# Performance work log

Hardware: AMD Instinct MI355X
Metric: run time of the kernel (lower is better)

## Reference

```python
import jax, jax.numpy as jnp
import numpy as np

K, N = 8192, 8192
GROUP_SIZE = 128
N_GROUPS = N // GROUP_SIZE  # 64
NBITS = 4
B, T = 8, 32


def setup_inputs() -> dict:
    key = jax.random.key(0)
    k_x, k_q, k_s, k_z, k_m1, k_m2, k_b = jax.random.split(key, 7)
    x = jax.random.normal(k_x, (B, T, N), dtype=jnp.float32)
    # int8 quantized weight codes in [0, 2**nbits - 1]
    W_q = jax.random.randint(k_q, (K, N), 0, 2 ** NBITS, dtype=jnp.int32)
    # group-wise scales/zeros, shaped for broadcast against [K, n_groups, group_size]
    scales = jax.random.uniform(k_s, (K, N_GROUPS, 1), dtype=jnp.float32, minval=0.01, maxval=0.1)
    zeros = jax.random.uniform(k_z, (K, N_GROUPS, 1), dtype=jnp.float32, minval=0.0, maxval=2.0 ** NBITS - 1.0)
    # Sinkhorn row/col scaling factors (positive, near 1)
    mu1 = jnp.exp(0.1 * jax.random.normal(k_m1, (N,), dtype=jnp.float32))
    mu2 = jnp.exp(0.1 * jax.random.normal(k_m2, (K,), dtype=jnp.float32))
    bias = jax.random.normal(k_b, (K,), dtype=jnp.float32)
    return {"x": x, "W_q": W_q, "scales": scales, "zeros": zeros,
            "mu1": mu1, "mu2": mu2, "bias": bias}


def reference(x, W_q, scales, zeros, mu1, mu2, bias):
    k, n = W_q.shape
    n_groups = scales.shape[1]
    group_size = n // n_groups
    # group-wise dequant: (Q - zero) * scale, then Sinkhorn row/col rescale
    Q_g = W_q.astype(jnp.float32).reshape(k, n_groups, group_size)
    W_deq = ((Q_g - zeros) * scales).reshape(k, n)
    W_deq = W_deq * mu2[:, None] * mu1[None, :]
    W_deq = W_deq.astype(x.dtype)
    # nn.functional.linear: x @ W^T + b ; x: [B, T, N] -> [B, T, K]
    out = jnp.einsum('btn,kn->btk', x, W_deq) + bias
    return out
```

## Files before the change

kernel.cpp:

```cpp
#include <hip/hip_runtime.h>
#include <hip/hip_bf16.h>

#define M_DIM 256
#define K_DIM 8192
#define N_DIM 8192
#define NGRP  64

#define BN 128
#define BK 32
#define THREADS 512
#define SPLITN 8
#define CHUNK  (N_DIM / SPLITN)
#define NSTEPS (CHUNK / BK)
#define NG     (CHUNK >> 7)

#define ASIZE 16384
#define BSIZE 8192
#define B_OFF  (3 * ASIZE)
#define SL_OFF (B_OFF + 2 * BSIZE)
#define LDS_TOTAL (SL_OFF + NG * 128 * 8)

typedef __bf16 bf16x8 __attribute__((ext_vector_type(8)));
typedef __bf16 bf16x4 __attribute__((ext_vector_type(4)));
typedef float  f32x4  __attribute__((ext_vector_type(4)));

#define SW(a) ((a) ^ ((((a) >> 7) & 7) << 4))

#define GLOAD_LDS16(g, l) __builtin_amdgcn_global_load_lds( \
    (const __attribute__((address_space(1))) void*)(g),     \
    (__attribute__((address_space(3))) void*)(l), 16, 0, 0)

__global__ __launch_bounds__(256) void prep_xs(const float* __restrict__ x,
                                               const float* __restrict__ mu1,
                                               __bf16* __restrict__ xs) {
    int t  = blockIdx.x * 256 + threadIdx.x;
    int n4 = t & 2047;
    int m  = t >> 11;
    int n  = n4 << 2;
    float4 xv = *(const float4*)(x + (size_t)m * N_DIM + n);
    float4 mv = *(const float4*)(mu1 + n);
    bf16x4 o;
    o[0] = (__bf16)(xv.x * mv.x);
    o[1] = (__bf16)(xv.y * mv.y);
    o[2] = (__bf16)(xv.z * mv.z);
    o[3] = (__bf16)(xv.w * mv.w);
    *(bf16x4*)(xs + (size_t)m * N_DIM + n) = o;
}

__global__ __launch_bounds__(THREADS, 4)
void gemm_q(const __bf16* __restrict__ xs, const int* __restrict__ Wq,
            const float* __restrict__ scales, const float* __restrict__ zeros,
            __bf16* __restrict__ partial) {
    extern __shared__ __align__(1024) char lds[];

    const int b     = blockIdx.x;
    const int split = b & 7;
    const int kidx  = b >> 3;
    const int k0    = kidx * BN;
    const int nbase = split * CHUNK;
    const int gbase = split * NG;

    const int tid  = threadIdx.x;
    const int lane = tid & 63;
    const int w    = tid >> 6;
    const int wmq  = w >> 1;
    const int wnh  = w & 1;
    const int start = kidx & (NSTEPS - 1);

    float* SL = (float*)(lds + SL_OFF);

    {
        int r = tid >> 2, gq = tid & 3;
#pragma unroll
        for (int gg = 0; gg < (NG >> 2); ++gg) {
            int g = (gg << 2) | gq;
            size_t si = (size_t)(k0 + r) * NGRP + gbase + g;
            float s = scales[si];
            float z = zeros[si];
            float2 v; v.x = s; v.y = -z * s;
            *(float2*)&SL[(size_t)((g << 7) + r) * 2] = v;
        }
    }
    asm volatile("s_waitcnt vmcnt(0) lgkmcnt(0)" ::: "memory");
    __builtin_amdgcn_s_barrier();

    const char* asrc[2];
    int aoff[2];
#pragma unroll
    for (int cc = 0; cc < 2; ++cc) {
        int c   = w * 2 + cc;
        int off = c * 1024 + lane * 16;
        int L   = SW(off);
        aoff[cc] = off;
        asrc[cc] = (const char*)xs + ((size_t)(L >> 6) * N_DIM) * 2 + (L & 63);
    }

    const int brow = w * 16 + (lane >> 2);
    const int bq   = lane & 3;
    const int* bptr0 = Wq + (size_t)(k0 + brow) * N_DIM + bq * 8;
    char* bdst0 = lds + B_OFF + SW(brow * 64 + bq * 16);

    int rb[4], ra[4];
#pragma unroll
    for (int i = 0; i < 4; ++i) {
        rb[i] = SW((wnh * 64 + i * 16 + (lane & 15)) * 64 + (lane >> 4) * 16);
        ra[i] = SW((wmq * 64 + i * 16 + (lane & 15)) * 64 + (lane >> 4) * 16);
    }

    char* pA0 = lds;
    char* pA1 = lds + ASIZE;
    char* pA2 = lds + 2 * ASIZE;

#define ISSUE_A(t, pbuf)                                                  \
    {                                                                     \
        int s_ = ((t) + start) & (NSTEPS - 1);                            \
        size_t so_ = (size_t)(nbase + s_ * BK) * 2;                       \
        GLOAD_LDS16(asrc[0] + so_, (pbuf) + aoff[0]);                     \
        GLOAD_LDS16(asrc[1] + so_, (pbuf) + aoff[1]);                     \
    }
#define LOAD_B(t, q0, q1)                                                 \
    {                                                                     \
        int s_ = ((t) + start) & (NSTEPS - 1);                            \
        const int* p_ = bptr0 + (nbase + s_ * BK);                        \
        q0 = *(const int4*)p_;                                            \
        q1 = *(const int4*)(p_ + 4);                                      \
    }

    f32x4 acc[4][4];
#pragma unroll
    for (int i = 0; i < 4; ++i)
#pragma unroll
        for (int j = 0; j < 4; ++j)
            acc[i][j] = (f32x4){0.f, 0.f, 0.f, 0.f};

    int4 qa0, qa1, qb0, qb1;

    LOAD_B(0, qa0, qa1);
    asm volatile("" ::: "memory");
    ISSUE_A(0, pA0);
    asm volatile("" ::: "memory");
    LOAD_B(1, qb0, qb1);
    asm volatile("" ::: "memory");
    ISSUE_A(1, pA1);

#define STEP(it, q0c, q1c, W1N, DO_ISS)                                   \
    {                                                                     \
        asm volatile("s_waitcnt vmcnt(" #W1N ")" ::: "memory");           \
        int scur_ = ((it) + start) & (NSTEPS - 1);                        \
        float2 sz_ = *(float2*)&SL[(size_t)(((scur_ >> 2) << 7) + brow) * 2]; \
        bf16x8 wv_;                                                       \
        wv_[0] = (__bf16)((float)q0c.x * sz_.x + sz_.y);                  \
        wv_[1] = (__bf16)((float)q0c.y * sz_.x + sz_.y);                  \
        wv_[2] = (__bf16)((float)q0c.z * sz_.x + sz_.y);                  \
        wv_[3] = (__bf16)((float)q0c.w * sz_.x + sz_.y);                  \
        wv_[4] = (__bf16)((float)q1c.x * sz_.x + sz_.y);                  \
        wv_[5] = (__bf16)((float)q1c.y * sz_.x + sz_.y);                  \
        wv_[6] = (__bf16)((float)q1c.z * sz_.x + sz_.y);                  \
        wv_[7] = (__bf16)((float)q1c.w * sz_.x + sz_.y);                  \
        *(bf16x8*)(bdst0 + ((it) & 1) * BSIZE) = wv_;                     \
        if (DO_ISS) { LOAD_B((it) + 2, q0c, q1c); }                       \
        asm volatile("s_waitcnt lgkmcnt(0)" ::: "memory");                \
        __builtin_amdgcn_s_barrier();                                     \
        const char* bufB_ = lds + B_OFF + ((it) & 1) * BSIZE;             \
        bf16x8 bv0_ = *(const bf16x8*)(bufB_ + rb[0]);                    \
        bf16x8 bv1_ = *(const bf16x8*)(bufB_ + rb[1]);                    \
        bf16x8 bv2_ = *(const bf16x8*)(bufB_ + rb[2]);                    \
        bf16x8 bv3_ = *(const bf16x8*)(bufB_ + rb[3]);                    \
        if (DO_ISS) { ISSUE_A((it) + 2, pA2); }                           \
        __builtin_amdgcn_s_setprio(1);                                    \
        _Pragma("unroll")                                                 \
        for (int mi = 0; mi < 4; ++mi) {                                  \
            bf16x8 av_ = *(const bf16x8*)(pA0 + ra[mi]);                  \
            acc[mi][0] = __builtin_amdgcn_mfma_f32_16x16x32_bf16(av_, bv0_, acc[mi][0], 0, 0, 0); \
            acc[mi][1] = __builtin_amdgcn_mfma_f32_16x16x32_bf16(av_, bv1_, acc[mi][1], 0, 0, 0); \
            acc[mi][2] = __builtin_amdgcn_mfma_f32_16x16x32_bf16(av_, bv2_, acc[mi][2], 0, 0, 0); \
            acc[mi][3] = __builtin_amdgcn_mfma_f32_16x16x32_bf16(av_, bv3_, acc[mi][3], 0, 0, 0); \
        }                                                                 \
        __builtin_amdgcn_s_setprio(0);                                    \
        { char* t_ = pA0; pA0 = pA1; pA1 = pA2; pA2 = t_; }               \
    }

    for (int it = 0; it < NSTEPS - 2; it += 2) {
        STEP(it,     qa0, qa1, 4, true);
        STEP(it + 1, qb0, qb1, 4, true);
    }
    STEP(NSTEPS - 2, qa0, qa1, 4, false);
    STEP(NSTEPS - 1, qb0, qb1, 0, false);
#undef STEP
#undef ISSUE_A
#undef LOAD_B

    __bf16* outp = partial + (size_t)split * ((size_t)M_DIM * K_DIM);
#pragma unroll
    for (int mi = 0; mi < 4; ++mi) {
#pragma unroll
        for (int ci = 0; ci < 4; ++ci) {
            int gk = k0 + wnh * 64 + ci * 16 + (lane & 15);
            int gm = wmq * 64 + mi * 16 + (lane >> 4) * 4;
#pragma unroll
            for (int rix = 0; rix < 4; ++rix)
                outp[(size_t)(gm + rix) * K_DIM + gk] = (__bf16)acc[mi][ci][rix];
        }
    }
}

__global__ __launch_bounds__(256) void reduce_out(const __bf16* __restrict__ partial,
                                                  const float* __restrict__ mu2,
                                                  const float* __restrict__ bias,
                                                  float* __restrict__ out) {
    int t  = blockIdx.x * 256 + threadIdx.x;
    int k4 = t & 2047;
    int m  = t >> 11;
    size_t base = (size_t)m * K_DIM + (size_t)k4 * 4;
    float4 s; s.x = 0.f; s.y = 0.f; s.z = 0.f; s.w = 0.f;
#pragma unroll
    for (int sp = 0; sp < SPLITN; ++sp) {
        bf16x4 p = *(const bf16x4*)(partial + (size_t)sp * ((size_t)M_DIM * K_DIM) + base);
        s.x += (float)p[0]; s.y += (float)p[1]; s.z += (float)p[2]; s.w += (float)p[3];
    }
    float4 m2 = *(const float4*)(mu2 + (size_t)k4 * 4);
    float4 bi = *(const float4*)(bias + (size_t)k4 * 4);
    float4 o;
    o.x = s.x * m2.x + bi.x;
    o.y = s.y * m2.y + bi.y;
    o.z = s.z * m2.z + bi.z;
    o.w = s.w * m2.w + bi.w;
    *(float4*)(out + base) = o;
}

extern "C" void kernel_launch(void* const* d_in, const int* in_sizes, int n_in,
                              void* d_out, int out_size, void* d_ws, size_t ws_size,
                              hipStream_t stream) {
    const float* x      = (const float*)d_in[0];
    const int*   Wq     = (const int*)d_in[1];
    const float* scales = (const float*)d_in[2];
    const float* zeros  = (const float*)d_in[3];
    const float* mu1    = (const float*)d_in[4];
    const float* mu2    = (const float*)d_in[5];
    const float* bias   = (const float*)d_in[6];
    float* out = (float*)d_out;

    __bf16* xs = (__bf16*)d_ws;
    const size_t xs_bytes = (size_t)M_DIM * N_DIM * sizeof(__bf16);
    __bf16* partial = (__bf16*)((char*)d_ws + xs_bytes);

    (void)hipFuncSetAttribute((const void*)gemm_q,
                              hipFuncAttributeMaxDynamicSharedMemorySize,
                              LDS_TOTAL);

    prep_xs<<<2048, 256, 0, stream>>>(x, mu1, xs);
    gemm_q<<<64 * SPLITN, THREADS, LDS_TOTAL, stream>>>(xs, Wq, scales, zeros, partial);
    reduce_out<<<2048, 256, 0, stream>>>(partial, mu2, bias, out);
}
```

Baseline: 84.67 us.

## Load quantized weight tiles in step pairs with nontemporal loads

The weight-code prefetch now loads two consecutive K-steps at a time (four 16-byte loads covering 64 contiguous ints per row) using nontemporal loads. The rotated start offset moves to pair granularity so each pair stays contiguous. The pipeline is restructured into a 4-step unrolled loop with adjusted vmcnt waits. The aim is fewer, larger memory requests and less cache pollution from the streaming weights, at the cost of more registers held for prefetched data.

```diff
diff --git a/kernel.cpp b/kernel.cpp
--- a/kernel.cpp
+++ b/kernel.cpp
@@ -12,6 +12,7 @@
 #define SPLITN 8
 #define CHUNK  (N_DIM / SPLITN)
 #define NSTEPS (CHUNK / BK)
+#define NPAIRS (NSTEPS / 2)
 #define NG     (CHUNK >> 7)
 
 #define ASIZE 16384
@@ -23,12 +24,17 @@
 typedef __bf16 bf16x8 __attribute__((ext_vector_type(8)));
 typedef __bf16 bf16x4 __attribute__((ext_vector_type(4)));
 typedef float  f32x4  __attribute__((ext_vector_type(4)));
+typedef int    i32x4  __attribute__((ext_vector_type(4)));
 
 #define SW(a) ((a) ^ ((((a) >> 7) & 7) << 4))
 
 #define GLOAD_LDS16(g, l) __builtin_amdgcn_global_load_lds( \
     (const __attribute__((address_space(1))) void*)(g),     \
     (__attribute__((address_space(3))) void*)(l), 16, 0, 0)
+
+#define NT4(p) __builtin_nontemporal_load((const i32x4*)(p))
+
+#define SMAP(t) (((((((t) >> 1) + startp) & (NPAIRS - 1))) << 1) | ((t) & 1))
 
 __global__ __launch_bounds__(256) void prep_xs(const float* __restrict__ x,
                                                const float* __restrict__ mu1,
@@ -65,7 +71,7 @@
     const int w    = tid >> 6;
     const int wmq  = w >> 1;
     const int wnh  = w & 1;
-    const int start = kidx & (NSTEPS - 1);
+    const int startp = kidx & (NPAIRS - 1);
 
     float* SL = (float*)(lds + SL_OFF);
 
@@ -113,17 +119,19 @@
 
 #define ISSUE_A(t, pbuf)                                                  \
     {                                                                     \
-        int s_ = ((t) + start) & (NSTEPS - 1);                            \
+        int s_ = SMAP(t);                                                 \
         size_t so_ = (size_t)(nbase + s_ * BK) * 2;                       \
         GLOAD_LDS16(asrc[0] + so_, (pbuf) + aoff[0]);                     \
         GLOAD_LDS16(asrc[1] + so_, (pbuf) + aoff[1]);                     \
     }
-#define LOAD_B(t, q0, q1)                                                 \
+#define LOAD_BPAIR(t, a0, a1, a2, a3)                                     \
     {                                                                     \
-        int s_ = ((t) + start) & (NSTEPS - 1);                            \
+        int s_ = SMAP(t);                                                 \
         const int* p_ = bptr0 + (nbase + s_ * BK);                        \
-        q0 = *(const int4*)p_;                                            \
-        q1 = *(const int4*)(p_ + 4);                                      \
+        a0 = NT4(p_);                                                     \
+        a1 = NT4(p_ + 4);                                                 \
+        a2 = NT4(p_ + 32);                                                \
+        a3 = NT4(p_ + 36);                                                \
     }
 
     f32x4 acc[4][4];
@@ -133,32 +141,32 @@
         for (int j = 0; j < 4; ++j)
             acc[i][j] = (f32x4){0.f, 0.f, 0.f, 0.f};
 
-    int4 qa0, qa1, qb0, qb1;
-
-    LOAD_B(0, qa0, qa1);
+    i32x4 pq0, pq1, pq2, pq3, rq0, rq1, rq2, rq3;
+
+    LOAD_BPAIR(0, pq0, pq1, pq2, pq3);
     asm volatile("" ::: "memory");
     ISSUE_A(0, pA0);
     asm volatile("" ::: "memory");
-    LOAD_B(1, qb0, qb1);
+    ISSUE_A(1, pA1);
     asm volatile("" ::: "memory");
-    ISSUE_A(1, pA1);
-
-#define STEP(it, q0c, q1c, W1N, DO_ISS)                                   \
+    LOAD_BPAIR(2, rq0, rq1, rq2, rq3);
+
+#define STEP(it, q0c, q1c, WSTR, BLOAD, DO_A)                             \
     {                                                                     \
-        asm volatile("s_waitcnt vmcnt(" #W1N ")" ::: "memory");           \
-        int scur_ = ((it) + start) & (NSTEPS - 1);                        \
+        asm volatile("s_waitcnt vmcnt(" WSTR ")" ::: "memory");           \
+        int scur_ = SMAP(it);                                             \
         float2 sz_ = *(float2*)&SL[(size_t)(((scur_ >> 2) << 7) + brow) * 2]; \
         bf16x8 wv_;                                                       \
-        wv_[0] = (__bf16)((float)q0c.x * sz_.x + sz_.y);                  \
-        wv_[1] = (__bf16)((float)q0c.y * sz_.x + sz_.y);                  \
-        wv_[2] = (__bf16)((float)q0c.z * sz_.x + sz_.y);                  \
-        wv_[3] = (__bf16)((float)q0c.w * sz_.x + sz_.y);                  \
-        wv_[4] = (__bf16)((float)q1c.x * sz_.x + sz_.y);                  \
-        wv_[5] = (__bf16)((float)q1c.y * sz_.x + sz_.y);                  \
-        wv_[6] = (__bf16)((float)q1c.z * sz_.x + sz_.y);                  \
-        wv_[7] = (__bf16)((float)q1c.w * sz_.x + sz_.y);                  \
+        wv_[0] = (__bf16)((float)q0c[0] * sz_.x + sz_.y);                 \
+        wv_[1] = (__bf16)((float)q0c[1] * sz_.x + sz_.y);                 \
+        wv_[2] = (__bf16)((float)q0c[2] * sz_.x + sz_.y);                 \
+        wv_[3] = (__bf16)((float)q0c[3] * sz_.x + sz_.y);                 \
+        wv_[4] = (__bf16)((float)q1c[0] * sz_.x + sz_.y);                 \
+        wv_[5] = (__bf16)((float)q1c[1] * sz_.x + sz_.y);                 \
+        wv_[6] = (__bf16)((float)q1c[2] * sz_.x + sz_.y);                 \
+        wv_[7] = (__bf16)((float)q1c[3] * sz_.x + sz_.y);                 \
         *(bf16x8*)(bdst0 + ((it) & 1) * BSIZE) = wv_;                     \
-        if (DO_ISS) { LOAD_B((it) + 2, q0c, q1c); }                       \
+        BLOAD;                                                            \
         asm volatile("s_waitcnt lgkmcnt(0)" ::: "memory");                \
         __builtin_amdgcn_s_barrier();                                     \
         const char* bufB_ = lds + B_OFF + ((it) & 1) * BSIZE;             \
@@ -166,7 +174,7 @@
         bf16x8 bv1_ = *(const bf16x8*)(bufB_ + rb[1]);                    \
         bf16x8 bv2_ = *(const bf16x8*)(bufB_ + rb[2]);                    \
         bf16x8 bv3_ = *(const bf16x8*)(bufB_ + rb[3]);                    \
-        if (DO_ISS) { ISSUE_A((it) + 2, pA2); }                           \
+        if (DO_A) { ISSUE_A((it) + 2, pA2); }                             \
         __builtin_amdgcn_s_setprio(1);                                    \
         _Pragma("unroll")                                                 \
         for (int mi = 0; mi < 4; ++mi) {                                  \
@@ -180,15 +188,21 @@
         { char* t_ = pA0; pA0 = pA1; pA1 = pA2; pA2 = t_; }               \
     }
 
-    for (int it = 0; it < NSTEPS - 2; it += 2) {
-        STEP(it,     qa0, qa1, 4, true);
-        STEP(it + 1, qb0, qb1, 4, true);
-    }
-    STEP(NSTEPS - 2, qa0, qa1, 4, false);
-    STEP(NSTEPS - 1, qb0, qb1, 0, false);
+#define NOB {}
+    for (int it = 0; it < NSTEPS - 4; it += 4) {
+        STEP(it,     pq0, pq1, "6", NOB, true);
+        STEP(it + 1, pq2, pq3, "6", LOAD_BPAIR((it) + 4, pq0, pq1, pq2, pq3), true);
+        STEP(it + 2, rq0, rq1, "6", NOB, true);
+        STEP(it + 3, rq2, rq3, "6", LOAD_BPAIR((it) + 6, rq0, rq1, rq2, rq3), true);
+    }
+    STEP(NSTEPS - 4, pq0, pq1, "6", NOB, true);
+    STEP(NSTEPS - 3, pq2, pq3, "6", NOB, true);
+    STEP(NSTEPS - 2, rq0, rq1, "2", NOB, false);
+    STEP(NSTEPS - 1, rq2, rq3, "0", NOB, false);
+#undef NOB
 #undef STEP
 #undef ISSUE_A
-#undef LOAD_B
+#undef LOAD_BPAIR
 
     __bf16* outp = partial + (size_t)split * ((size_t)M_DIM * K_DIM);
 #pragma unroll
```

Result: slower. 167.0 us (+97.2%).

## Halve K-tile to 64 with 256-thread blocks and single-buffer A tile

Applied to the files above, without the earlier changes.

Shrinks each GEMM block from 128 to 64 output columns with 4 waves, doubling the grid to 1024 blocks, and replaces the triple-buffered A (activation) tile in LDS with a single buffer plus an extra barrier before reissuing the next A load. The aim is lower LDS use and more blocks to fill the CUs. In exchange, the activation tile is reloaded twice as often across blocks, and the single-buffered A serializes the A load with compute, which reduces overlap.

```diff
diff --git a/kernel.cpp b/kernel.cpp
--- a/kernel.cpp
+++ b/kernel.cpp
@@ -6,19 +6,19 @@
 #define N_DIM 8192
 #define NGRP  64
 
-#define BN 128
+#define BN 64
 #define BK 32
-#define THREADS 512
+#define THREADS 256
 #define SPLITN 8
 #define CHUNK  (N_DIM / SPLITN)
 #define NSTEPS (CHUNK / BK)
 #define NG     (CHUNK >> 7)
 
 #define ASIZE 16384
-#define BSIZE 8192
-#define B_OFF  (3 * ASIZE)
-#define SL_OFF (B_OFF + 2 * BSIZE)
-#define LDS_TOTAL (SL_OFF + NG * 128 * 8)
+#define BSIZE 4096
+#define B_OFF  ASIZE
+#define SL_OFF (ASIZE + 2 * BSIZE)
+#define LDS_TOTAL (SL_OFF + NG * 64 * 8)
 
 typedef __bf16 bf16x8 __attribute__((ext_vector_type(8)));
 typedef __bf16 bf16x4 __attribute__((ext_vector_type(4)));
@@ -63,60 +63,56 @@
     const int tid  = threadIdx.x;
     const int lane = tid & 63;
     const int w    = tid >> 6;
-    const int wmq  = w >> 1;
-    const int wnh  = w & 1;
     const int start = kidx & (NSTEPS - 1);
 
     float* SL = (float*)(lds + SL_OFF);
 
     {
-        int r = tid >> 2, gq = tid & 3;
-#pragma unroll
-        for (int gg = 0; gg < (NG >> 2); ++gg) {
-            int g = (gg << 2) | gq;
+        int e0 = tid;
+        int e1 = tid + 256;
+#pragma unroll
+        for (int pass = 0; pass < 2; ++pass) {
+            int e = pass ? e1 : e0;
+            int r = e & 63, g = e >> 6;
             size_t si = (size_t)(k0 + r) * NGRP + gbase + g;
             float s = scales[si];
             float z = zeros[si];
             float2 v; v.x = s; v.y = -z * s;
-            *(float2*)&SL[(size_t)((g << 7) + r) * 2] = v;
+            *(float2*)&SL[(size_t)((g << 6) + r) * 2] = v;
         }
     }
     asm volatile("s_waitcnt vmcnt(0) lgkmcnt(0)" ::: "memory");
     __builtin_amdgcn_s_barrier();
 
-    const char* asrc[2];
-    int aoff[2];
-#pragma unroll
-    for (int cc = 0; cc < 2; ++cc) {
-        int c   = w * 2 + cc;
-        int off = c * 1024 + lane * 16;
+    const char* asrc[4];
+    int aoff[4];
+#pragma unroll
+    for (int cc = 0; cc < 4; ++cc) {
+        int off = cc * 4096 + tid * 16;
         int L   = SW(off);
         aoff[cc] = off;
         asrc[cc] = (const char*)xs + ((size_t)(L >> 6) * N_DIM) * 2 + (L & 63);
     }
 
-    const int brow = w * 16 + (lane >> 2);
-    const int bq   = lane & 3;
+    const int brow = tid >> 2;
+    const int bq   = tid & 3;
     const int* bptr0 = Wq + (size_t)(k0 + brow) * N_DIM + bq * 8;
     char* bdst0 = lds + B_OFF + SW(brow * 64 + bq * 16);
 
     int rb[4], ra[4];
 #pragma unroll
     for (int i = 0; i < 4; ++i) {
-        rb[i] = SW((wnh * 64 + i * 16 + (lane & 15)) * 64 + (lane >> 4) * 16);
-        ra[i] = SW((wmq * 64 + i * 16 + (lane & 15)) * 64 + (lane >> 4) * 16);
-    }
-
-    char* pA0 = lds;
-    char* pA1 = lds + ASIZE;
-    char* pA2 = lds + 2 * ASIZE;
-
-#define ISSUE_A(t, pbuf)                                                  \
+        rb[i] = SW((i * 16 + (lane & 15)) * 64 + (lane >> 4) * 16);
+        ra[i] = SW((w * 64 + i * 16 + (lane & 15)) * 64 + (lane >> 4) * 16);
+    }
+
+#define ISSUE_A(t)                                                        \
     {                                                                     \
         int s_ = ((t) + start) & (NSTEPS - 1);                            \
         size_t so_ = (size_t)(nbase + s_ * BK) * 2;                       \
-        GLOAD_LDS16(asrc[0] + so_, (pbuf) + aoff[0]);                     \
-        GLOAD_LDS16(asrc[1] + so_, (pbuf) + aoff[1]);                     \
+        _Pragma("unroll")                                                 \
+        for (int cc = 0; cc < 4; ++cc)                                    \
+            GLOAD_LDS16(asrc[cc] + so_, lds + aoff[cc]);                  \
     }
 #define LOAD_B(t, q0, q1)                                                 \
     {                                                                     \
@@ -137,17 +133,15 @@
 
     LOAD_B(0, qa0, qa1);
     asm volatile("" ::: "memory");
-    ISSUE_A(0, pA0);
-    asm volatile("" ::: "memory");
     LOAD_B(1, qb0, qb1);
     asm volatile("" ::: "memory");
-    ISSUE_A(1, pA1);
-
-#define STEP(it, q0c, q1c, W1N, DO_ISS)                                   \
+    ISSUE_A(0);
+    asm volatile("s_waitcnt vmcnt(6)" ::: "memory");
+
+#define STEP(it, q0c, q1c, WSTR, DO_B, DO_A)                              \
     {                                                                     \
-        asm volatile("s_waitcnt vmcnt(" #W1N ")" ::: "memory");           \
         int scur_ = ((it) + start) & (NSTEPS - 1);                        \
-        float2 sz_ = *(float2*)&SL[(size_t)(((scur_ >> 2) << 7) + brow) * 2]; \
+        float2 sz_ = *(float2*)&SL[(size_t)(((scur_ >> 2) << 6) + brow) * 2]; \
         bf16x8 wv_;                                                       \
         wv_[0] = (__bf16)((float)q0c.x * sz_.x + sz_.y);                  \
         wv_[1] = (__bf16)((float)q0c.y * sz_.x + sz_.y);                  \
@@ -158,34 +152,34 @@
         wv_[6] = (__bf16)((float)q1c.z * sz_.x + sz_.y);                  \
         wv_[7] = (__bf16)((float)q1c.w * sz_.x + sz_.y);                  \
         *(bf16x8*)(bdst0 + ((it) & 1) * BSIZE) = wv_;                     \
-        if (DO_ISS) { LOAD_B((it) + 2, q0c, q1c); }                       \
-        asm volatile("s_waitcnt lgkmcnt(0)" ::: "memory");                \
+        if (DO_B) { LOAD_B((it) + 2, q0c, q1c); }                         \
+        asm volatile("s_waitcnt vmcnt(" WSTR ") lgkmcnt(0)" ::: "memory"); \
         __builtin_amdgcn_s_barrier();                                     \
         const char* bufB_ = lds + B_OFF + ((it) & 1) * BSIZE;             \
         bf16x8 bv0_ = *(const bf16x8*)(bufB_ + rb[0]);                    \
         bf16x8 bv1_ = *(const bf16x8*)(bufB_ + rb[1]);                    \
         bf16x8 bv2_ = *(const bf16x8*)(bufB_ + rb[2]);                    \
         bf16x8 bv3_ = *(const bf16x8*)(bufB_ + rb[3]);                    \
-        if (DO_ISS) { ISSUE_A((it) + 2, pA2); }                           \
         __builtin_amdgcn_s_setprio(1);                                    \
         _Pragma("unroll")                                                 \
         for (int mi = 0; mi < 4; ++mi) {                                  \
-            bf16x8 av_ = *(const bf16x8*)(pA0 + ra[mi]);                  \
+            bf16x8 av_ = *(const bf16x8*)(lds + ra[mi]);                  \
             acc[mi][0] = __builtin_amdgcn_mfma_f32_16x16x32_bf16(av_, bv0_, acc[mi][0], 0, 0, 0); \
             acc[mi][1] = __builtin_amdgcn_mfma_f32_16x16x32_bf16(av_, bv1_, acc[mi][1], 0, 0, 0); \
             acc[mi][2] = __builtin_amdgcn_mfma_f32_16x16x32_bf16(av_, bv2_, acc[mi][2], 0, 0, 0); \
             acc[mi][3] = __builtin_amdgcn_mfma_f32_16x16x32_bf16(av_, bv3_, acc[mi][3], 0, 0, 0); \
         }                                                                 \
         __builtin_amdgcn_s_setprio(0);                                    \
-        { char* t_ = pA0; pA0 = pA1; pA1 = pA2; pA2 = t_; }               \
+        __builtin_amdgcn_s_barrier();                                     \
+        if (DO_A) { ISSUE_A((it) + 1); }                                  \
     }
 
     for (int it = 0; it < NSTEPS - 2; it += 2) {
-        STEP(it,     qa0, qa1, 4, true);
-        STEP(it + 1, qb0, qb1, 4, true);
-    }
-    STEP(NSTEPS - 2, qa0, qa1, 4, false);
-    STEP(NSTEPS - 1, qb0, qb1, 0, false);
+        STEP(it,     qa0, qa1, "2", true, true);
+        STEP(it + 1, qb0, qb1, "2", true, true);
+    }
+    STEP(NSTEPS - 2, qa0, qa1, "0", false, true);
+    STEP(NSTEPS - 1, qb0, qb1, "0", false, false);
 #undef STEP
 #undef ISSUE_A
 #undef LOAD_B
@@ -195,8 +189,8 @@
     for (int mi = 0; mi < 4; ++mi) {
 #pragma unroll
         for (int ci = 0; ci < 4; ++ci) {
-            int gk = k0 + wnh * 64 + ci * 16 + (lane & 15);
-            int gm = wmq * 64 + mi * 16 + (lane >> 4) * 4;
+            int gk = k0 + ci * 16 + (lane & 15);
+            int gm = w * 64 + mi * 16 + (lane >> 4) * 4;
 #pragma unroll
             for (int rix = 0; rix < 4; ++rix)
                 outp[(size_t)(gm + rix) * K_DIM + gk] = (__bf16)acc[mi][ci][rix];
@@ -249,6 +243,6 @@
                               LDS_TOTAL);
 
     prep_xs<<<2048, 256, 0, stream>>>(x, mu1, xs);
-    gemm_q<<<64 * SPLITN, THREADS, LDS_TOTAL, stream>>>(xs, Wq, scales, zeros, partial);
+    gemm_q<<<(K_DIM / BN) * SPLITN, THREADS, LDS_TOTAL, stream>>>(xs, Wq, scales, zeros, partial);
     reduce_out<<<2048, 256, 0, stream>>>(partial, mu2, bias, out);
 }
```

Result: slower. 112.3 us (+32.6%).
